# Performance work log

Hardware: AMD Instinct MI355X
Metric: run time of the kernel (lower is better)

## Reference

```python
import jax, jax.numpy as jnp
import numpy as np

B, S, E = 32, 577, 1024
H = 16
D = E // H  # head_size = 64


def setup_inputs() -> dict:
    key = jax.random.key(0)
    ks = jax.random.split(key, 5)
    scale_init = E ** -0.5
    x = jax.random.normal(ks[0], (B, S, E), dtype=jnp.float32)
    # Per-head projection weights. torch Linear weight is [out,in]; we store
    # [H, E, D] so that x @ Wq[h] == torch_linear(x) with weight Wq[h].T.
    Wq = jax.random.normal(ks[1], (H, E, D), dtype=jnp.float32) * scale_init
    Wk = jax.random.normal(ks[2], (H, E, D), dtype=jnp.float32) * scale_init
    Wv = jax.random.normal(ks[3], (H, E, D), dtype=jnp.float32) * scale_init
    # Output projection (with bias, as in nn.Linear default)
    Wo = jax.random.normal(ks[4], (E, E), dtype=jnp.float32) * scale_init
    bo = jnp.zeros((E,), dtype=jnp.float32)
    return {"x": x, "Wq": Wq, "Wk": Wk, "Wv": Wv, "Wo": Wo, "bo": bo}


def reference(x, Wq, Wk, Wv, Wo, bo):
    scale = D ** -0.5
    # Per-head QKV projections, vectorized over heads: [B,H,S,D]
    q = jnp.einsum('bse,hed->bhsd', x, Wq)
    k = jnp.einsum('bse,hed->bhsd', x, Wk)
    v = jnp.einsum('bse,hed->bhsd', x, Wv)
    scores = jnp.einsum('bhsd,bhtd->bhst', q, k) * scale  # [B,H,S,S]
    attn = jax.nn.softmax(scores, axis=-1)
    out = jnp.einsum('bhst,bhtd->bhsd', attn, v)  # [B,H,S,D]
    # Concat heads: head h occupies slice [h*D:(h+1)*D], matching torch.cat order
    out = out.transpose(0, 2, 1, 3).reshape(B, S, E)
    return out @ Wo.T + bo  # torch Linear: x @ W.T + b
```

## Files before the change

kernel.cpp:

```cpp
#include <hip/hip_runtime.h>
#include <hip/hip_bf16.h>
#include <stdint.h>

using sh8    = __attribute__((ext_vector_type(8))) short;
using f32x4  = __attribute__((ext_vector_type(4))) float;
using f32x16 = __attribute__((ext_vector_type(16))) float;

#define MFMA16(a, b, c) __builtin_amdgcn_mfma_f32_16x16x32_bf16(a, b, c, 0, 0, 0)
#define MFMA32(a, b, c) __builtin_amdgcn_mfma_f32_32x32x16_bf16(a, b, c, 0, 0, 0)
#define EXP2F(x) __builtin_amdgcn_exp2f(x)

static constexpr int BB = 32, SS = 577, HH = 16;
static constexpr int MM = BB * SS;
static constexpr int SPAD = 640;
static constexpr float QSCALE = 0.18033688011112042f;

__device__ __forceinline__ ushort f2b(float f) {
  union { float f; uint32_t u; } v{f};
  uint32_t r = v.u + 0x7FFFu + ((v.u >> 16) & 1u);
  return (ushort)(r >> 16);
}

#if __has_builtin(__builtin_amdgcn_cvt_pk_bf16_f32)
typedef __attribute__((ext_vector_type(2))) __bf16 bf16x2_t;
__device__ __forceinline__ uint32_t pk_bf16(float a, float b) {
  union { bf16x2_t v; uint32_t u; } c;
  c.v = __builtin_amdgcn_cvt_pk_bf16_f32(a, b);
  return c.u;
}
#else
__device__ __forceinline__ uint32_t pk_bf16(float a, float b) {
  return (uint32_t)f2b(a) | ((uint32_t)f2b(b) << 16);
}
#endif

__device__ __forceinline__ void gld16(const ushort* g, ushort* l) {
  __builtin_amdgcn_global_load_lds(
      (const __attribute__((address_space(1))) uint32_t*)g,
      (__attribute__((address_space(3))) uint32_t*)l, 16, 0, 0);
}

__global__ __launch_bounds__(256)
void convert2_f32_bf16(const float* __restrict__ a, ushort* __restrict__ oa, int na4,
                       const float* __restrict__ b, ushort* __restrict__ ob, int nb4) {
  const int total = na4 + nb4;
  const int stride = gridDim.x * 256;
  for (int i = blockIdx.x * 256 + threadIdx.x; i < total; i += stride) {
    const float4 f = (i < na4) ? ((const float4*)a)[i] : ((const float4*)b)[i - na4];
    ushort4 u;
    u.x = f2b(f.x); u.y = f2b(f.y); u.z = f2b(f.z); u.w = f2b(f.w);
    if (i < na4) ((ushort4*)oa)[i] = u;
    else         ((ushort4*)ob)[i - na4] = u;
  }
}

__global__ __launch_bounds__(256)
void convert_wqkv(const float* __restrict__ Wq, const float* __restrict__ Wk,
                  const float* __restrict__ Wv, ushort* __restrict__ Wt) {
  __shared__ ushort T[64 * 72];
  const int tid = threadIdx.x;
  const int kt = blockIdx.x, sh = blockIdx.y;
  const int sel = sh >> 4, h = sh & 15;
  const float* W = (sel == 0) ? Wq : ((sel == 1) ? Wk : Wv);
  const float qs = (sel == 0) ? QSCALE : 1.0f;
  const int rr = tid >> 4;
  const int rc = (tid & 15) * 4;
#pragma unroll
  for (int p = 0; p < 64; p += 16) {
    const float4 f = *(const float4*)(W + (size_t)h * 65536 + (size_t)(kt * 64 + p + rr) * 64 + rc);
    ushort4 u;
    u.x = f2b(f.x * qs); u.y = f2b(f.y * qs); u.z = f2b(f.z * qs); u.w = f2b(f.w * qs);
    *(ushort4*)&T[(p + rr) * 72 + rc] = u;
  }
  __syncthreads();
  const int dd = tid >> 2;
  const int c16 = (tid & 3) * 16;
  sh8 v0, v1;
#pragma unroll
  for (int j = 0; j < 8; j++) v0[j] = (short)T[(c16 + j) * 72 + dd];
#pragma unroll
  for (int j = 0; j < 8; j++) v1[j] = (short)T[(c16 + 8 + j) * 72 + dd];
  ushort* op = Wt + ((size_t)sel * 1024 + h * 64 + dd) * 1024 + kt * 64 + c16;
  *(sh8*)op = v0;
  *(sh8*)(op + 8) = v1;
}

template <int MODE>
__global__ __launch_bounds__(256)
void gemm_bt(const ushort* __restrict__ A, const ushort* __restrict__ Bt,
             ushort* __restrict__ Cb, float* __restrict__ Cf,
             const float* __restrict__ bias, int M, int N, int K) {
  __shared__ ushort Al[128 * 64];
  __shared__ ushort Bl[128 * 64];
  const int tid = threadIdx.x;
  const int lane = tid & 63, w = tid >> 6;
  const int l31 = lane & 31, hw = lane >> 5;
  const int wm = (w >> 1) * 64, wn = (w & 1) * 64;
  const int m0 = blockIdx.y * 128, n0 = blockIdx.x * 128;

  f32x16 acc[2][2];
#pragma unroll
  for (int i = 0; i < 2; i++)
#pragma unroll
    for (int j = 0; j < 2; j++)
#pragma unroll
      for (int r = 0; r < 16; r++) acc[i][j][r] = 0.f;

  const int rbase = tid >> 3;
  const int swzc = ((tid & 7) ^ (rbase & 7)) * 8;
  const ushort* Ag[4]; const ushort* Bg[4];
  ushort* lA[4]; ushort* lB[4];
#pragma unroll
  for (int i = 0; i < 4; i++) {
    Ag[i] = A + (size_t)min(m0 + i * 32 + rbase, M - 1) * K + swzc;
    Bg[i] = Bt + (size_t)(n0 + i * 32 + rbase) * K + swzc;
    lA[i] = &Al[(i * 256 + tid) * 8];
    lB[i] = &Bl[(i * 256 + tid) * 8];
  }
  const int swz = l31 & 7;
  int ck[4];
#pragma unroll
  for (int ks = 0; ks < 4; ks++) ck[ks] = ((ks * 2 + hw) ^ swz) * 8;

  for (int k0 = 0; k0 < K; k0 += 64) {
    __syncthreads();
#pragma unroll
    for (int i = 0; i < 4; i++) {
      gld16(Ag[i] + k0, lA[i]);
      gld16(Bg[i] + k0, lB[i]);
    }
    __syncthreads();
#pragma unroll
    for (int ks = 0; ks < 4; ks++) {
      sh8 af[2], bf[2];
#pragma unroll
      for (int i = 0; i < 2; i++) af[i] = *(const sh8*)&Al[(wm + i * 32 + l31) * 64 + ck[ks]];
#pragma unroll
      for (int j = 0; j < 2; j++) bf[j] = *(const sh8*)&Bl[(wn + j * 32 + l31) * 64 + ck[ks]];
#pragma unroll
      for (int i = 0; i < 2; i++)
#pragma unroll
        for (int j = 0; j < 2; j++) acc[i][j] = MFMA32(bf[j], af[i], acc[i][j]);
    }
  }

#pragma unroll
  for (int i = 0; i < 2; i++) {
    const int row = m0 + wm + i * 32 + l31;
    const bool ok = row < M;
#pragma unroll
    for (int j = 0; j < 2; j++) {
#pragma unroll
      for (int rg = 0; rg < 4; rg++) {
        const int col0 = n0 + wn + j * 32 + rg * 8 + hw * 4;
        if (MODE == 0) {
          uint2 pk;
          pk.x = pk_bf16(acc[i][j][rg * 4 + 0], acc[i][j][rg * 4 + 1]);
          pk.y = pk_bf16(acc[i][j][rg * 4 + 2], acc[i][j][rg * 4 + 3]);
          if (ok) *(uint2*)&Cb[(size_t)row * N + col0] = pk;
        } else {
          const float4 b4 = *(const float4*)&bias[col0];
          float4 v;
          v.x = acc[i][j][rg * 4 + 0] + b4.x; v.y = acc[i][j][rg * 4 + 1] + b4.y;
          v.z = acc[i][j][rg * 4 + 2] + b4.z; v.w = acc[i][j][rg * 4 + 3] + b4.w;
          if (ok) *(float4*)&Cf[(size_t)row * N + col0] = v;
        }
      }
    }
  }
}

__global__ __launch_bounds__(256)
void transpose_v(const ushort* __restrict__ QKV, ushort* __restrict__ Vtg) {
  __shared__ ushort T[64 * 72];
  const int tid = threadIdx.x;
  const int st = blockIdx.x, bh = blockIdx.y;
  const int b = bh >> 4, h = bh & 15;
  const int sr = tid >> 3;
  const int sc = (tid & 7) * 8;
#pragma unroll
  for (int p = 0; p < 64; p += 32) {
    const int s = st * 64 + p + sr;
    uint4 d = uint4{0u, 0u, 0u, 0u};
    if (s < SS) d = *(const uint4*)(QKV + ((size_t)b * SS + s) * 3072 + 2048 + h * 64 + sc);
    *(uint4*)&T[(p + sr) * 72 + sc] = d;
  }
  __syncthreads();
  const int dd = tid >> 2;
  const int s16 = (tid & 3) * 16;
  sh8 v0, v1;
#pragma unroll
  for (int j = 0; j < 8; j++) v0[j] = (short)T[(s16 + j) * 72 + dd];
#pragma unroll
  for (int j = 0; j < 8; j++) v1[j] = (short)T[(s16 + 8 + j) * 72 + dd];
  ushort* outp = Vtg + ((size_t)bh * 64 + dd) * SPAD + st * 64 + s16;
  *(sh8*)outp = v0;
  *(sh8*)(outp + 8) = v1;
}

__global__ __launch_bounds__(256)
void flash_attn(const ushort* __restrict__ QKV, const ushort* __restrict__ Vtg,
                ushort* __restrict__ Ob) {
  __shared__ ushort Kl[64 * 64];
  __shared__ ushort Vl[64 * 64];
  __shared__ ushort Pl[128 * 72];
  const int tid = threadIdx.x;
  const int lane = tid & 63, w = tid >> 6;
  const int l15 = lane & 15, quad = lane >> 4;
  const int qb = blockIdx.x, bh = blockIdx.y;
  const int b = bh >> 4, h = bh & 15;

  sh8 qf[2][2];
#pragma unroll
  for (int g = 0; g < 2; g++) {
    const int qr = qb * 128 + w * 32 + g * 16 + l15;
    const ushort* qrow = QKV + ((size_t)b * SS + min(qr, SS - 1)) * 3072 + h * 64;
    qf[g][0] = *(const sh8*)(qrow + quad * 8);
    qf[g][1] = *(const sh8*)(qrow + 32 + quad * 8);
  }

  sh8 ones;
#pragma unroll
  for (int j = 0; j < 8; j++) ones[j] = (short)0x3F80;

  f32x4 o[2][4];
  f32x4 acc_l[2];
#pragma unroll
  for (int g = 0; g < 2; g++) {
    acc_l[g] = f32x4{0.f, 0.f, 0.f, 0.f};
#pragma unroll
    for (int t = 0; t < 4; t++) o[g][t] = f32x4{0.f, 0.f, 0.f, 0.f};
  }

  const int r0 = tid >> 3;
  const int swzs = ((tid & 7) ^ (r0 & 7)) * 8;
  const ushort* Kg = QKV + (size_t)b * SS * 3072 + 1024 + h * 64 + swzs;
  const ushort* Vg0 = Vtg + ((size_t)bh * 64 + r0) * SPAD + swzs;
  const ushort* Vg1 = Vtg + ((size_t)bh * 64 + 32 + r0) * SPAD + swzs;
  ushort* lK0 = &Kl[tid * 8];
  ushort* lK1 = &Kl[(256 + tid) * 8];
  ushort* lV0 = &Vl[tid * 8];
  ushort* lV1 = &Vl[(256 + tid) * 8];

  const int swz = l15 & 7;
  const int ca0 = (quad ^ swz) * 8;
  const int ca1 = ((quad + 4) ^ swz) * 8;
  ushort* plw[2] = { &Pl[(w * 32 + l15) * 72], &Pl[(w * 32 + 16 + l15) * 72] };

  for (int kt = 0; kt < 10; kt++) {
    const int kb = kt * 64;
    __syncthreads();
    gld16(Kg + (size_t)min(kb + r0, SS - 1) * 3072, lK0);
    gld16(Kg + (size_t)min(kb + 32 + r0, SS - 1) * 3072, lK1);
    gld16(Vg0 + kb, lV0);
    gld16(Vg1 + kb, lV1);
    __syncthreads();

#pragma unroll
    for (int tn = 0; tn < 4; tn++) {
      const int kr = tn * 16 + l15;
      const sh8 k0 = *(const sh8*)&Kl[kr * 64 + ca0];
      const sh8 k1 = *(const sh8*)&Kl[kr * 64 + ca1];
#pragma unroll
      for (int g = 0; g < 2; g++) {
        f32x4 s = f32x4{0.f, 0.f, 0.f, 0.f};
        s = MFMA16(k0, qf[g][0], s);
        s = MFMA16(k1, qf[g][1], s);
        if (kt == 9) {
#pragma unroll
          for (int r = 0; r < 4; r++)
            if ((tn * 16 + quad * 4 + r) != 0) s[r] = -1e30f;
        }
        uint2 pp;
        pp.x = pk_bf16(EXP2F(s[0]), EXP2F(s[1]));
        pp.y = pk_bf16(EXP2F(s[2]), EXP2F(s[3]));
        *(uint2*)(plw[g] + tn * 16 + quad * 4) = pp;
      }
    }
    sh8 pa[2][2];
#pragma unroll
    for (int g = 0; g < 2; g++) {
      pa[g][0] = *(const sh8*)(plw[g] + quad * 8);
      pa[g][1] = *(const sh8*)(plw[g] + 32 + quad * 8);
      acc_l[g] = MFMA16(ones, pa[g][0], acc_l[g]);
      acc_l[g] = MFMA16(ones, pa[g][1], acc_l[g]);
    }
#pragma unroll
    for (int t = 0; t < 4; t++) {
      const int vr = t * 16 + l15;
      const sh8 v0 = *(const sh8*)&Vl[vr * 64 + ca0];
      const sh8 v1 = *(const sh8*)&Vl[vr * 64 + ca1];
#pragma unroll
      for (int g = 0; g < 2; g++) {
        o[g][t] = MFMA16(v0, pa[g][0], o[g][t]);
        o[g][t] = MFMA16(v1, pa[g][1], o[g][t]);
      }
    }
  }

#pragma unroll
  for (int g = 0; g < 2; g++) {
    const float inv = 1.0f / acc_l[g][0];
    const int s = qb * 128 + w * 32 + g * 16 + l15;
    if (s < SS) {
      ushort* op = Ob + ((size_t)b * SS + s) * 1024 + h * 64 + quad * 4;
#pragma unroll
      for (int t = 0; t < 4; t++) {
        uint2 ov;
        ov.x = pk_bf16(o[g][t][0] * inv, o[g][t][1] * inv);
        ov.y = pk_bf16(o[g][t][2] * inv, o[g][t][3] * inv);
        *(uint2*)(op + t * 16) = ov;
      }
    }
  }
}

extern "C" void kernel_launch(void* const* d_in, const int* in_sizes, int n_in,
                              void* d_out, int out_size, void* d_ws, size_t ws_size,
                              hipStream_t stream) {
  const float* x  = (const float*)d_in[0];
  const float* Wq = (const float*)d_in[1];
  const float* Wk = (const float*)d_in[2];
  const float* Wv = (const float*)d_in[3];
  const float* Wo = (const float*)d_in[4];
  const float* bo = (const float*)d_in[5];
  float* out = (float*)d_out;

  ushort* Xb  = (ushort*)d_ws;
  ushort* Wt  = Xb  + (size_t)MM * 1024;
  ushort* Wob = Wt  + (size_t)3072 * 1024;
  ushort* QKV = Wob + (size_t)1024 * 1024;
  ushort* Vtg = QKV + (size_t)MM * 3072;
  ushort* Ob  = Xb;

  convert2_f32_bf16<<<4096, 256, 0, stream>>>(x, Xb, MM * 1024 / 4, Wo, Wob, 1024 * 1024 / 4);
  convert_wqkv<<<dim3(16, 48), 256, 0, stream>>>(Wq, Wk, Wv, Wt);
  gemm_bt<0><<<dim3(24, 145), 256, 0, stream>>>(Xb, Wt, QKV, nullptr, nullptr, MM, 3072, 1024);
  transpose_v<<<dim3(10, 512), 256, 0, stream>>>(QKV, Vtg);
  flash_attn<<<dim3(5, 512), 256, 0, stream>>>(QKV, Vtg, Ob);
  gemm_bt<1><<<dim3(8, 145), 256, 0, stream>>>(Ob, Wob, nullptr, out, bo, MM, 1024, 1024);
}
```

Measured before the change: 454.3 us.

## Replace 128x128 GEMM with double-buffered 256x256 8-wave GEMM and XCD remap

```diff
diff --git a/kernel.cpp b/kernel.cpp
--- a/kernel.cpp
+++ b/kernel.cpp
@@ -7,8 +7,11 @@
 using f32x16 = __attribute__((ext_vector_type(16))) float;
 
 #define MFMA16(a, b, c) __builtin_amdgcn_mfma_f32_16x16x32_bf16(a, b, c, 0, 0, 0)
-#define MFMA32(a, b, c) __builtin_amdgcn_mfma_f32_32x32x16_bf16(a, b, c, 0, 0, 0)
 #define EXP2F(x) __builtin_amdgcn_exp2f(x)
+#define SBAR()  __builtin_amdgcn_s_barrier()
+#define PRIO1() __builtin_amdgcn_s_setprio(1)
+#define PRIO0() __builtin_amdgcn_s_setprio(0)
+#define WAITL() asm volatile("s_waitcnt lgkmcnt(0)" ::: "memory")
 
 static constexpr int BB = 32, SS = 577, HH = 16;
 static constexpr int MM = BB * SS;
@@ -86,85 +89,156 @@
 }
 
 template <int MODE>
-__global__ __launch_bounds__(256)
-void gemm_bt(const ushort* __restrict__ A, const ushort* __restrict__ Bt,
+__global__ __launch_bounds__(512, 2)
+void gemm256(const ushort* __restrict__ A, const ushort* __restrict__ Bt,
              ushort* __restrict__ Cb, float* __restrict__ Cf,
-             const float* __restrict__ bias, int M, int N, int K) {
-  __shared__ ushort Al[128 * 64];
-  __shared__ ushort Bl[128 * 64];
+             const float* __restrict__ bias, int N) {
+  constexpr int K = 1024;
+  constexpr int NT = K / 64;
+  __shared__ ushort Al[2][256 * 64];
+  __shared__ ushort Bl[2][256 * 64];
   const int tid = threadIdx.x;
-  const int lane = tid & 63, w = tid >> 6;
-  const int l31 = lane & 31, hw = lane >> 5;
-  const int wm = (w >> 1) * 64, wn = (w & 1) * 64;
-  const int m0 = blockIdx.y * 128, n0 = blockIdx.x * 128;
-
-  f32x16 acc[2][2];
-#pragma unroll
-  for (int i = 0; i < 2; i++)
-#pragma unroll
-    for (int j = 0; j < 2; j++)
-#pragma unroll
-      for (int r = 0; r < 16; r++) acc[i][j][r] = 0.f;
-
-  const int rbase = tid >> 3;
-  const int swzc = ((tid & 7) ^ (rbase & 7)) * 8;
-  const ushort* Ag[4]; const ushort* Bg[4];
-  ushort* lA[4]; ushort* lB[4];
-#pragma unroll
-  for (int i = 0; i < 4; i++) {
-    Ag[i] = A + (size_t)min(m0 + i * 32 + rbase, M - 1) * K + swzc;
-    Bg[i] = Bt + (size_t)(n0 + i * 32 + rbase) * K + swzc;
-    lA[i] = &Al[(i * 256 + tid) * 8];
-    lB[i] = &Bl[(i * 256 + tid) * 8];
-  }
-  const int swz = l31 & 7;
-  int ck[4];
-#pragma unroll
-  for (int ks = 0; ks < 4; ks++) ck[ks] = ((ks * 2 + hw) ^ swz) * 8;
-
-  for (int k0 = 0; k0 < K; k0 += 64) {
-    __syncthreads();
+  const int lane = tid & 63;
+  const int w = tid >> 6;
+  const int l15 = lane & 15, quad = lane >> 4;
+  const int wm = (w >> 2) * 128;
+  const int wn = (w & 3) * 64;
+
+  const int nwg = gridDim.x * gridDim.y;
+  const int orig = blockIdx.y * gridDim.x + blockIdx.x;
+  const int q = nwg >> 3, r = nwg & 7;
+  const int xcd = orig & 7, loc = orig >> 3;
+  const int wgid = (xcd < r ? xcd * (q + 1) : r * (q + 1) + (xcd - r) * q) + loc;
+  const int m0 = (wgid / gridDim.x) * 256;
+  const int n0 = (wgid % gridDim.x) * 256;
+
+  f32x4 acc[8][4];
+#pragma unroll
+  for (int i = 0; i < 8; i++)
+#pragma unroll
+    for (int j = 0; j < 4; j++) acc[i][j] = f32x4{0.f, 0.f, 0.f, 0.f};
+
+  const int r9 = tid >> 3;
+  const int cs = ((tid & 7) ^ (r9 & 7)) * 8;
+  const ushort* Asrc[4];
+#pragma unroll
+  for (int i = 0; i < 4; i++)
+    Asrc[i] = A + (size_t)min(m0 + i * 64 + r9, MM - 1) * K + cs;
+  const ushort* Bsrc = Bt + (size_t)(n0 + r9) * K + cs;
+  ushort* dA = &Al[0][0] + tid * 8;
+  ushort* dB = &Bl[0][0] + tid * 8;
+
+#define STG_A(i, b, kt) gld16(Asrc[i] + (kt) * 64, dA + (b) * 16384 + (i) * 4096)
+#define STG_B(i, b, kt) gld16(Bsrc + (size_t)(i) * (64 * 1024) + (kt) * 64, dB + (b) * 16384 + (i) * 4096)
+
+  const int swz = l15 & 7;
+  const int c0 = (quad ^ swz) * 8;
+  const int c1 = ((quad + 4) ^ swz) * 8;
+  const int arow = (wm + l15) * 64;
+  const int brow = (wn + l15) * 64;
+
+#pragma unroll
+  for (int i = 0; i < 4; i++) { STG_A(i, 0, 0); STG_B(i, 0, 0); }
+#pragma unroll
+  for (int i = 0; i < 4; i++) { STG_A(i, 1, 1); STG_B(i, 1, 1); }
+  asm volatile("s_waitcnt vmcnt(8)" ::: "memory");
+  SBAR();
+
+  sh8 af[4][2], bf[4][2];
+  for (int t = 0; t < NT; ++t) {
+    const ushort* Ab = &Al[t & 1][0];
+    const ushort* Bb = &Bl[t & 1][0];
+    const int pb = t & 1;
+    const bool st = (t < NT - 2);
+    const int kt = t + 2;
+
 #pragma unroll
     for (int i = 0; i < 4; i++) {
-      gld16(Ag[i] + k0, lA[i]);
-      gld16(Bg[i] + k0, lB[i]);
-    }
-    __syncthreads();
-#pragma unroll
-    for (int ks = 0; ks < 4; ks++) {
-      sh8 af[2], bf[2];
-#pragma unroll
-      for (int i = 0; i < 2; i++) af[i] = *(const sh8*)&Al[(wm + i * 32 + l31) * 64 + ck[ks]];
-#pragma unroll
-      for (int j = 0; j < 2; j++) bf[j] = *(const sh8*)&Bl[(wn + j * 32 + l31) * 64 + ck[ks]];
-#pragma unroll
-      for (int i = 0; i < 2; i++)
-#pragma unroll
-        for (int j = 0; j < 2; j++) acc[i][j] = MFMA32(bf[j], af[i], acc[i][j]);
-    }
-  }
-
-#pragma unroll
-  for (int i = 0; i < 2; i++) {
-    const int row = m0 + wm + i * 32 + l31;
-    const bool ok = row < M;
+      af[i][0] = *(const sh8*)(Ab + arow + i * 1024 + c0);
+      af[i][1] = *(const sh8*)(Ab + arow + i * 1024 + c1);
+    }
 #pragma unroll
     for (int j = 0; j < 2; j++) {
-#pragma unroll
-      for (int rg = 0; rg < 4; rg++) {
-        const int col0 = n0 + wn + j * 32 + rg * 8 + hw * 4;
-        if (MODE == 0) {
-          uint2 pk;
-          pk.x = pk_bf16(acc[i][j][rg * 4 + 0], acc[i][j][rg * 4 + 1]);
-          pk.y = pk_bf16(acc[i][j][rg * 4 + 2], acc[i][j][rg * 4 + 3]);
-          if (ok) *(uint2*)&Cb[(size_t)row * N + col0] = pk;
-        } else {
-          const float4 b4 = *(const float4*)&bias[col0];
-          float4 v;
-          v.x = acc[i][j][rg * 4 + 0] + b4.x; v.y = acc[i][j][rg * 4 + 1] + b4.y;
-          v.z = acc[i][j][rg * 4 + 2] + b4.z; v.w = acc[i][j][rg * 4 + 3] + b4.w;
-          if (ok) *(float4*)&Cf[(size_t)row * N + col0] = v;
-        }
+      bf[j][0] = *(const sh8*)(Bb + brow + j * 1024 + c0);
+      bf[j][1] = *(const sh8*)(Bb + brow + j * 1024 + c1);
+    }
+    SBAR(); WAITL(); PRIO1();
+#pragma unroll
+    for (int i = 0; i < 4; i++)
+#pragma unroll
+      for (int j = 0; j < 2; j++) {
+        acc[i][j] = MFMA16(bf[j][0], af[i][0], acc[i][j]);
+        acc[i][j] = MFMA16(bf[j][1], af[i][1], acc[i][j]);
+      }
+    PRIO0(); SBAR();
+
+#pragma unroll
+    for (int j = 2; j < 4; j++) {
+      bf[j][0] = *(const sh8*)(Bb + brow + j * 1024 + c0);
+      bf[j][1] = *(const sh8*)(Bb + brow + j * 1024 + c1);
+    }
+    if (st) { STG_A(0, pb, kt); STG_A(2, pb, kt); }
+    SBAR(); WAITL(); PRIO1();
+#pragma unroll
+    for (int i = 0; i < 4; i++)
+#pragma unroll
+      for (int j = 2; j < 4; j++) {
+        acc[i][j] = MFMA16(bf[j][0], af[i][0], acc[i][j]);
+        acc[i][j] = MFMA16(bf[j][1], af[i][1], acc[i][j]);
+      }
+    PRIO0(); SBAR();
+
+#pragma unroll
+    for (int i = 0; i < 4; i++) {
+      af[i][0] = *(const sh8*)(Ab + arow + (i + 4) * 1024 + c0);
+      af[i][1] = *(const sh8*)(Ab + arow + (i + 4) * 1024 + c1);
+    }
+    if (st) { STG_B(0, pb, kt); STG_B(1, pb, kt); STG_B(2, pb, kt); STG_B(3, pb, kt); }
+    SBAR(); WAITL(); PRIO1();
+#pragma unroll
+    for (int i = 0; i < 4; i++)
+#pragma unroll
+      for (int j = 2; j < 4; j++) {
+        acc[i + 4][j] = MFMA16(bf[j][0], af[i][0], acc[i + 4][j]);
+        acc[i + 4][j] = MFMA16(bf[j][1], af[i][1], acc[i + 4][j]);
+      }
+    PRIO0(); SBAR();
+
+    if (st) { STG_A(1, pb, kt); STG_A(3, pb, kt); }
+    SBAR(); PRIO1();
+#pragma unroll
+    for (int i = 0; i < 4; i++)
+#pragma unroll
+      for (int j = 0; j < 2; j++) {
+        acc[i + 4][j] = MFMA16(bf[j][0], af[i][0], acc[i + 4][j]);
+        acc[i + 4][j] = MFMA16(bf[j][1], af[i][1], acc[i + 4][j]);
+      }
+    PRIO0();
+    if (st) { asm volatile("s_waitcnt vmcnt(8)" ::: "memory"); }
+    else    { asm volatile("s_waitcnt vmcnt(0)" ::: "memory"); }
+    SBAR();
+  }
+#undef STG_A
+#undef STG_B
+
+#pragma unroll
+  for (int i = 0; i < 8; i++) {
+    const int row = m0 + wm + i * 16 + l15;
+    const bool ok = row < MM;
+#pragma unroll
+    for (int j = 0; j < 4; j++) {
+      const int col0 = n0 + wn + j * 16 + quad * 4;
+      if (MODE == 0) {
+        uint2 pk;
+        pk.x = pk_bf16(acc[i][j][0], acc[i][j][1]);
+        pk.y = pk_bf16(acc[i][j][2], acc[i][j][3]);
+        if (ok) *(uint2*)&Cb[(size_t)row * N + col0] = pk;
+      } else {
+        const float4 b4 = *(const float4*)&bias[col0];
+        float4 v;
+        v.x = acc[i][j][0] + b4.x; v.y = acc[i][j][1] + b4.y;
+        v.z = acc[i][j][2] + b4.z; v.w = acc[i][j][3] + b4.w;
+        if (ok) *(float4*)&Cf[(size_t)row * N + col0] = v;
       }
     }
   }
@@ -335,8 +409,8 @@
 
   convert2_f32_bf16<<<4096, 256, 0, stream>>>(x, Xb, MM * 1024 / 4, Wo, Wob, 1024 * 1024 / 4);
   convert_wqkv<<<dim3(16, 48), 256, 0, stream>>>(Wq, Wk, Wv, Wt);
-  gemm_bt<0><<<dim3(24, 145), 256, 0, stream>>>(Xb, Wt, QKV, nullptr, nullptr, MM, 3072, 1024);
+  gemm256<0><<<dim3(12, 73), 512, 0, stream>>>(Xb, Wt, QKV, nullptr, nullptr, 3072);
   transpose_v<<<dim3(10, 512), 256, 0, stream>>>(QKV, Vtg);
   flash_attn<<<dim3(5, 512), 256, 0, stream>>>(QKV, Vtg, Ob);
-  gemm_bt<1><<<dim3(8, 145), 256, 0, stream>>>(Ob, Wob, nullptr, out, bo, MM, 1024, 1024);
-}
+  gemm256<1><<<dim3(4, 73), 512, 0, stream>>>(Ob, Wob, nullptr, out, bo, 1024);
+}
```

Result: no change. 459.8 us (+1.2%).

## Replace GEMM with 256x256 double-buffered tiles and XCD-aware block remap

Applied to the files above, without the earlier changes.

```diff
diff --git a/kernel.cpp b/kernel.cpp
--- a/kernel.cpp
+++ b/kernel.cpp
@@ -9,6 +9,8 @@
 #define MFMA16(a, b, c) __builtin_amdgcn_mfma_f32_16x16x32_bf16(a, b, c, 0, 0, 0)
 #define MFMA32(a, b, c) __builtin_amdgcn_mfma_f32_32x32x16_bf16(a, b, c, 0, 0, 0)
 #define EXP2F(x) __builtin_amdgcn_exp2f(x)
+#define SBAR()  __builtin_amdgcn_s_barrier()
+#define CFENCE() asm volatile("" ::: "memory")
 
 static constexpr int BB = 32, SS = 577, HH = 16;
 static constexpr int MM = BB * SS;
@@ -86,68 +88,100 @@
 }
 
 template <int MODE>
-__global__ __launch_bounds__(256)
-void gemm_bt(const ushort* __restrict__ A, const ushort* __restrict__ Bt,
+__global__ __launch_bounds__(512, 2)
+void gemm256(const ushort* __restrict__ A, const ushort* __restrict__ Bt,
              ushort* __restrict__ Cb, float* __restrict__ Cf,
-             const float* __restrict__ bias, int M, int N, int K) {
-  __shared__ ushort Al[128 * 64];
-  __shared__ ushort Bl[128 * 64];
+             const float* __restrict__ bias, int N) {
+  constexpr int K = 1024;
+  constexpr int NT = K / 64;
+  __shared__ ushort Al[2][256 * 64];
+  __shared__ ushort Bl[2][256 * 64];
   const int tid = threadIdx.x;
-  const int lane = tid & 63, w = tid >> 6;
+  const int lane = tid & 63;
+  const int w = tid >> 6;
   const int l31 = lane & 31, hw = lane >> 5;
-  const int wm = (w >> 1) * 64, wn = (w & 1) * 64;
-  const int m0 = blockIdx.y * 128, n0 = blockIdx.x * 128;
-
-  f32x16 acc[2][2];
-#pragma unroll
-  for (int i = 0; i < 2; i++)
+  const int wm = (w >> 2) * 128;
+  const int wn = (w & 3) * 64;
+
+  const int nwg = gridDim.x * gridDim.y;
+  const int orig = blockIdx.y * gridDim.x + blockIdx.x;
+  const int q = nwg >> 3, r = nwg & 7;
+  const int xcd = orig & 7, loc = orig >> 3;
+  const int wgid = (xcd < r ? xcd * (q + 1) : r * (q + 1) + (xcd - r) * q) + loc;
+  const int m0 = (wgid / gridDim.x) * 256;
+  const int n0 = (wgid % gridDim.x) * 256;
+
+  f32x16 acc[4][2];
+#pragma unroll
+  for (int i = 0; i < 4; i++)
 #pragma unroll
     for (int j = 0; j < 2; j++)
 #pragma unroll
-      for (int r = 0; r < 16; r++) acc[i][j][r] = 0.f;
-
-  const int rbase = tid >> 3;
-  const int swzc = ((tid & 7) ^ (rbase & 7)) * 8;
-  const ushort* Ag[4]; const ushort* Bg[4];
-  ushort* lA[4]; ushort* lB[4];
+      for (int rg = 0; rg < 16; rg++) acc[i][j][rg] = 0.f;
+
+  const int r9 = tid >> 3;
+  const int cs = ((tid & 7) ^ (r9 & 7)) * 8;
+  const ushort* Asrc[4];
+  const ushort* Bsrc[4];
 #pragma unroll
   for (int i = 0; i < 4; i++) {
-    Ag[i] = A + (size_t)min(m0 + i * 32 + rbase, M - 1) * K + swzc;
-    Bg[i] = Bt + (size_t)(n0 + i * 32 + rbase) * K + swzc;
-    lA[i] = &Al[(i * 256 + tid) * 8];
-    lB[i] = &Bl[(i * 256 + tid) * 8];
-  }
+    Asrc[i] = A + (size_t)min(m0 + i * 64 + r9, MM - 1) * K + cs;
+    Bsrc[i] = Bt + (size_t)(n0 + i * 64 + r9) * K + cs;
+  }
+  ushort* dA = &Al[0][0] + tid * 8;
+  ushort* dB = &Bl[0][0] + tid * 8;
+
+#define STAGE(b, ko)                                              \
+  do {                                                            \
+    _Pragma("unroll")                                             \
+    for (int i_ = 0; i_ < 4; i_++) {                              \
+      gld16(Asrc[i_] + (ko), dA + (b) * 16384 + i_ * 4096);       \
+      gld16(Bsrc[i_] + (ko), dB + (b) * 16384 + i_ * 4096);       \
+    }                                                             \
+  } while (0)
+
   const int swz = l31 & 7;
   int ck[4];
 #pragma unroll
   for (int ks = 0; ks < 4; ks++) ck[ks] = ((ks * 2 + hw) ^ swz) * 8;
-
-  for (int k0 = 0; k0 < K; k0 += 64) {
-    __syncthreads();
-#pragma unroll
-    for (int i = 0; i < 4; i++) {
-      gld16(Ag[i] + k0, lA[i]);
-      gld16(Bg[i] + k0, lB[i]);
-    }
-    __syncthreads();
+  const int arow = (wm + l31) * 64;
+  const int brow = (wn + l31) * 64;
+
+  STAGE(0, 0);
+  asm volatile("s_waitcnt vmcnt(0)" ::: "memory");
+  SBAR();
+  CFENCE();
+
+  for (int t = 0; t < NT; ++t) {
+    const ushort* Ab = &Al[t & 1][0];
+    const ushort* Bb = &Bl[t & 1][0];
+    if (t < NT - 1) STAGE((t + 1) & 1, (t + 1) * 64);
+
 #pragma unroll
     for (int ks = 0; ks < 4; ks++) {
-      sh8 af[2], bf[2];
-#pragma unroll
-      for (int i = 0; i < 2; i++) af[i] = *(const sh8*)&Al[(wm + i * 32 + l31) * 64 + ck[ks]];
-#pragma unroll
-      for (int j = 0; j < 2; j++) bf[j] = *(const sh8*)&Bl[(wn + j * 32 + l31) * 64 + ck[ks]];
-#pragma unroll
-      for (int i = 0; i < 2; i++)
+      sh8 af[4], bf[2];
+#pragma unroll
+      for (int i = 0; i < 4; i++) af[i] = *(const sh8*)(Ab + arow + i * 2048 + ck[ks]);
+#pragma unroll
+      for (int j = 0; j < 2; j++) bf[j] = *(const sh8*)(Bb + brow + j * 2048 + ck[ks]);
+#pragma unroll
+      for (int i = 0; i < 4; i++)
 #pragma unroll
         for (int j = 0; j < 2; j++) acc[i][j] = MFMA32(bf[j], af[i], acc[i][j]);
     }
-  }
-
-#pragma unroll
-  for (int i = 0; i < 2; i++) {
+
+    if (t < NT - 1) {
+      asm volatile("s_waitcnt vmcnt(0)" ::: "memory");
+      SBAR();
+      CFENCE();
+    }
+  }
+#undef STAGE
+
+#pragma unroll
+  for (int i = 0; i < 4; i++) {
     const int row = m0 + wm + i * 32 + l31;
-    const bool ok = row < M;
+    const bool ok = row < MM;
 #pragma unroll
     for (int j = 0; j < 2; j++) {
 #pragma unroll
@@ -335,8 +369,8 @@
 
   convert2_f32_bf16<<<4096, 256, 0, stream>>>(x, Xb, MM * 1024 / 4, Wo, Wob, 1024 * 1024 / 4);
   convert_wqkv<<<dim3(16, 48), 256, 0, stream>>>(Wq, Wk, Wv, Wt);
-  gemm_bt<0><<<dim3(24, 145), 256, 0, stream>>>(Xb, Wt, QKV, nullptr, nullptr, MM, 3072, 1024);
+  gemm256<0><<<dim3(12, 73), 512, 0, stream>>>(Xb, Wt, QKV, nullptr, nullptr, 3072);
   transpose_v<<<dim3(10, 512), 256, 0, stream>>>(QKV, Vtg);
   flash_attn<<<dim3(5, 512), 256, 0, stream>>>(QKV, Vtg, Ob);
-  gemm_bt<1><<<dim3(8, 145), 256, 0, stream>>>(Ob, Wob, nullptr, out, bo, MM, 1024, 1024);
-}
+  gemm256<1><<<dim3(4, 73), 512, 0, stream>>>(Ob, Wob, nullptr, out, bo, 1024);
+}
```

Result: slower. 464.8 us (+2.3%).
